# Optimization experiments

Hardware: AMD Instinct MI355X
Metric: run time of the kernel (lower is better)

Reference implementation:

```python
import jax, jax.numpy as jnp
import numpy as np

N, E, H, L, G = 50000, 500000, 128, 4, 1000
EPS = 1e-7      # GENConv message eps
LN_EPS = 1e-5   # torch LayerNorm default


def setup_inputs() -> dict:
    key = jax.random.key(0)
    ks = jax.random.split(key, 24)
    d = {}
    d["x"] = jax.random.normal(ks[0], (N, 9), jnp.float32)
    d["edge_index"] = jax.random.randint(ks[1], (2, E), 0, N, jnp.int32)
    d["edge_attr"] = jax.random.normal(ks[2], (E, 3), jnp.float32)
    d["batch"] = jnp.sort(jax.random.randint(ks[3], (N,), 0, G, jnp.int32))
    s9, s3, sh, s2h = 1/np.sqrt(9), 1/np.sqrt(3), 1/np.sqrt(H), 1/np.sqrt(2*H)
    u = lambda k, shp, s: jax.random.uniform(k, shp, jnp.float32, -s, s)
    d["enc_node_W"] = u(ks[4], (9, H), s9)
    d["enc_node_b"] = u(ks[5], (H,), s9)
    d["enc_edge_W"] = u(ks[6], (3, H), s3)
    d["enc_edge_b"] = u(ks[7], (H,), s3)
    d["ln_g"] = jnp.ones((L, H), jnp.float32)   # DeepGCNLayer pre-norm affine
    d["ln_b"] = jnp.zeros((L, H), jnp.float32)
    d["W1"] = u(ks[8], (L, H, 2*H), sh)          # GENConv MLP layer 1
    d["b1"] = u(ks[9], (L, 2*H), sh)
    d["mlp_ln_g"] = jnp.ones((L, 2*H), jnp.float32)
    d["mlp_ln_b"] = jnp.zeros((L, 2*H), jnp.float32)
    d["W2"] = u(ks[10], (L, 2*H, H), s2h)        # GENConv MLP layer 2
    d["b2"] = u(ks[11], (L, H), s2h)
    d["t"] = jnp.ones((L,), jnp.float32)         # learnable softmax temperature, init 1.0
    return d


def layernorm(x, g, b):
    mu = x.mean(-1, keepdims=True)
    var = ((x - mu) ** 2).mean(-1, keepdims=True)
    return (x - mu) / jnp.sqrt(var + LN_EPS) * g + b


def genconv(h, src, dst, ea, t, W1, b1, lg, lb, W2, b2):
    # message: relu(x_j + edge_attr) + eps   -> [E, H]
    msg = jax.nn.relu(h[src] + ea) + EPS
    # softmax aggregation over incoming edges, per channel
    logits = t * msg
    m = jax.ops.segment_max(logits, dst, num_segments=N)
    num = jnp.exp(logits - m[dst])
    den = jax.ops.segment_sum(num, dst, num_segments=N)
    alpha = num / den[dst]
    agg = jax.ops.segment_sum(msg * alpha, dst, num_segments=N)
    out = agg + h  # root residual inside GENConv
    z = jax.nn.relu(layernorm(out @ W1 + b1, lg, lb))
    return z @ W2 + b2


def reference(x, edge_index, edge_attr, batch, enc_node_W, enc_node_b,
              enc_edge_W, enc_edge_b, ln_g, ln_b, W1, b1, mlp_ln_g, mlp_ln_b,
              W2, b2, t):
    src, dst = edge_index[0], edge_index[1]
    h = x @ enc_node_W + enc_node_b            # node encoder  [N, H]
    ea = edge_attr @ enc_edge_W + enc_edge_b   # edge encoder  [E, H]
    # layer 0: conv only (DeeperGCN forward uses layers[0].conv directly)
    h = genconv(h, src, dst, ea, t[0], W1[0], b1[0], mlp_ln_g[0], mlp_ln_b[0], W2[0], b2[0])
    # layers 1..L-1: res+ block: x + conv(relu(LN(x))); dropout is identity (eval)
    for i in range(1, L):
        z = jax.nn.relu(layernorm(h, ln_g[i], ln_b[i]))
        h = h + genconv(z, src, dst, ea, t[i], W1[i], b1[i], mlp_ln_g[i], mlp_ln_b[i], W2[i], b2[i])
    h = jax.nn.relu(layernorm(h, ln_g[0], ln_b[0]))  # reuses layer-0 norm
    # global mean pool over graphs
    counts = jax.ops.segment_sum(jnp.ones((N,), h.dtype), batch, num_segments=G)
    sums = jax.ops.segment_sum(h, batch, num_segments=G)
    return sums / jnp.maximum(counts, 1.0)[:, None]
```

## Files before the change

### kernel.cpp

```cpp
#include <hip/hip_runtime.h>

#define NN 50000
#define NE 500000
#define HD 128
#define HD2 256
#define NL 4
#define NG 1000

constexpr float MSG_EPS = 1e-7f;
constexpr float LNEPS   = 1e-5f;

typedef float  f32x4  __attribute__((ext_vector_type(4)));
typedef float  f32x2  __attribute__((ext_vector_type(2)));
typedef __bf16 bf16x8 __attribute__((ext_vector_type(8)));

__device__ __forceinline__ unsigned short f2b(float f) {
    unsigned int u = __float_as_uint(f);
    unsigned int r = u + 0x7FFFu + ((u >> 16) & 1u);
    return (unsigned short)(r >> 16);
}
__device__ __forceinline__ float b2f(unsigned short h) {
    return __uint_as_float(((unsigned int)h) << 16);
}
__device__ __forceinline__ unsigned int pack2(float a, float b) {
    return (unsigned int)f2b(a) | ((unsigned int)f2b(b) << 16);
}

#define PREP_BLKS 512
#define ENC_BLKS 25000
#define HIST_BLKS ((NE + 255) / 256)

__global__ void k_setup(const float* __restrict__ x, const float* __restrict__ encW,
                        const float* __restrict__ encB, unsigned short* __restrict__ zb,
                        const float* __restrict__ W1, const float* __restrict__ W2,
                        unsigned short* __restrict__ W1T, unsigned short* __restrict__ W2T,
                        const int* __restrict__ dst, int* __restrict__ counts) {
    int bid = blockIdx.x, tid = threadIdx.x;
    if (bid < PREP_BLKS) {
        int idx = bid * 256 + tid;
        {
            int k = idx & 127, n = (idx >> 7) & 255, l = idx >> 15;
            W1T[idx] = f2b(W1[(l * 128 + k) * 256 + n]);
        }
        {
            int k = idx & 255, n = (idx >> 8) & 127, l = idx >> 15;
            W2T[idx] = f2b(W2[(l * 256 + k) * 128 + n]);
        }
    } else if (bid < PREP_BLKS + ENC_BLKS) {
        int n = (bid - PREP_BLKS) * 2 + (tid >> 7);
        int c = tid & 127;
        float xr[9];
#pragma unroll
        for (int k = 0; k < 9; k++) xr[k] = x[n * 9 + k];
        float acc = encB[c];
#pragma unroll
        for (int k = 0; k < 9; k++) acc = fmaf(xr[k], encW[k * HD + c], acc);
        zb[(size_t)n * HD + c] = f2b(acc);
    } else {
        int e = (bid - PREP_BLKS - ENC_BLKS) * 256 + tid;
        if (e < NE) atomicAdd(&counts[dst[e]], 1);
    }
}

#define SCAN_B 512
#define NSB ((NN + SCAN_B - 1) / SCAN_B)

__global__ void k_scan1(const int* __restrict__ counts, int* __restrict__ incl,
                        int* __restrict__ bsum) {
    __shared__ int s[SCAN_B];
    int i = blockIdx.x * SCAN_B + threadIdx.x;
    int v = (i < NN) ? counts[i] : 0;
    s[threadIdx.x] = v;
    __syncthreads();
    for (int off = 1; off < SCAN_B; off <<= 1) {
        int t = (threadIdx.x >= off) ? s[threadIdx.x - off] : 0;
        __syncthreads();
        s[threadIdx.x] += t;
        __syncthreads();
    }
    if (i < NN) incl[i] = s[threadIdx.x];
    if (threadIdx.x == SCAN_B - 1) bsum[blockIdx.x] = s[threadIdx.x];
}

__global__ void k_scan2(const int* __restrict__ bsum, int* __restrict__ boff, int nb) {
    __shared__ int s[128];
    int v = (threadIdx.x < nb) ? bsum[threadIdx.x] : 0;
    s[threadIdx.x] = v;
    __syncthreads();
    for (int off = 1; off < 128; off <<= 1) {
        int t = (threadIdx.x >= off) ? s[threadIdx.x - off] : 0;
        __syncthreads();
        s[threadIdx.x] += t;
        __syncthreads();
    }
    if (threadIdx.x < nb) boff[threadIdx.x] = s[threadIdx.x] - v;
}

__global__ void k_scan3g(const int* __restrict__ incl, const int* __restrict__ boff,
                         int* __restrict__ row_start, const int* __restrict__ batch,
                         int* __restrict__ gstart) {
    if (blockIdx.x < NSB) {
        int i = blockIdx.x * SCAN_B + threadIdx.x;
        if (i < NN) row_start[i + 1] = incl[i] + boff[blockIdx.x];
        if (i == 0) row_start[0] = 0;
    } else {
        int g = (blockIdx.x - NSB) * SCAN_B + threadIdx.x;
        if (g > NG) return;
        int lo = 0, hi = NN;
        while (lo < hi) {
            int mid = (lo + hi) >> 1;
            if (batch[mid] < g) lo = mid + 1;
            else hi = mid;
        }
        gstart[g] = lo;
    }
}

__global__ void k_scatter(const int* __restrict__ src, const int* __restrict__ dst,
                          const float* __restrict__ eattr, const int* __restrict__ row_start,
                          int* __restrict__ cursor, float4* __restrict__ aperm) {
    int e = blockIdx.x * blockDim.x + threadIdx.x;
    if (e >= NE) return;
    int d = dst[e];
    int p = row_start[d] + atomicAdd(&cursor[d], 1);
    float4 v;
    v.x = eattr[e * 3 + 0];
    v.y = eattr[e * 3 + 1];
    v.z = eattr[e * 3 + 2];
    v.w = __int_as_float(src[e]);
    aperm[p] = v;
}

__device__ __forceinline__ void edge_acc2(float4 a, unsigned int zz, f32x2 w0, f32x2 w1,
                                          f32x2 w2, f32x2 bb, float tv, f32x2& num,
                                          f32x2& wm) {
    f32x2 z;
    z.x = b2f((unsigned short)zz);
    z.y = b2f((unsigned short)(zz >> 16));
    f32x2 m = z + bb + a.x * w0 + a.y * w1 + a.z * w2;
    m.x = fmaxf(m.x, 0.f);
    m.y = fmaxf(m.y, 0.f);
    f32x2 tm = tv * m;
    f32x2 e;
    e.x = __expf(tm.x);
    e.y = __expf(tm.y);
    num += e;
    wm += m * e;
}

__global__ __launch_bounds__(256) void k_aggregate(const unsigned short* __restrict__ zbin,
                                                   const float4* __restrict__ aperm,
                                                   const int* __restrict__ row_start,
                                                   const float* __restrict__ We,
                                                   const float* __restrict__ be,
                                                   const float* __restrict__ t, int layer,
                                                   unsigned int* __restrict__ outb) {
    int w = threadIdx.x >> 6, lane = threadIdx.x & 63;
    int n = blockIdx.x * 4 + w;
    if (n >= NN) return;
    int c = lane * 2;
    f32x2 w0 = *(const f32x2*)&We[c];
    f32x2 w1 = *(const f32x2*)&We[HD + c];
    f32x2 w2 = *(const f32x2*)&We[2 * HD + c];
    f32x2 bb = *(const f32x2*)&be[c];
    float tv = t[layer];
    int s0 = row_start[n], s1 = row_start[n + 1];
    f32x2 num = (f32x2){0.f, 0.f}, wm = (f32x2){0.f, 0.f};
    const unsigned int* z32 = (const unsigned int*)zbin;
    int p = s0;
    for (; p + 8 <= s1; p += 8) {
        float4 A[8];
#pragma unroll
        for (int j = 0; j < 8; j++) A[j] = aperm[p + j];
        unsigned int Z[8];
#pragma unroll
        for (int j = 0; j < 8; j++) {
            int sj = __builtin_amdgcn_readfirstlane(__float_as_int(A[j].w));
            Z[j] = z32[(size_t)sj * 64 + lane];
        }
#pragma unroll
        for (int j = 0; j < 8; j++) edge_acc2(A[j], Z[j], w0, w1, w2, bb, tv, num, wm);
    }
    for (; p + 4 <= s1; p += 4) {
        float4 A[4];
#pragma unroll
        for (int j = 0; j < 4; j++) A[j] = aperm[p + j];
        unsigned int Z[4];
#pragma unroll
        for (int j = 0; j < 4; j++) {
            int sj = __builtin_amdgcn_readfirstlane(__float_as_int(A[j].w));
            Z[j] = z32[(size_t)sj * 64 + lane];
        }
#pragma unroll
        for (int j = 0; j < 4; j++) edge_acc2(A[j], Z[j], w0, w1, w2, bb, tv, num, wm);
    }
    for (; p < s1; p++) {
        float4 a = aperm[p];
        int sj = __builtin_amdgcn_readfirstlane(__float_as_int(a.w));
        unsigned int zz = z32[(size_t)sj * 64 + lane];
        edge_acc2(a, zz, w0, w1, w2, bb, tv, num, wm);
    }
    unsigned int zn = z32[(size_t)n * 64 + lane];
    bool has = s1 > s0;
    float ox = (has ? (wm.x / num.x + MSG_EPS) : 0.f) + b2f((unsigned short)zn);
    float oy = (has ? (wm.y / num.y + MSG_EPS) : 0.f) + b2f((unsigned short)(zn >> 16));
    outb[(size_t)n * 64 + lane] = pack2(ox, oy);
}

#define BM 32
#define HS_LD 264
#define HT_LD 136

__global__ __launch_bounds__(256) void k_mlp(const unsigned short* __restrict__ outb,
                                             const unsigned short* __restrict__ W1T,
                                             const float* __restrict__ b1l,
                                             const float* __restrict__ lgl,
                                             const float* __restrict__ lbl,
                                             const unsigned short* __restrict__ W2T,
                                             const float* __restrict__ b2l,
                                             unsigned short* __restrict__ h,
                                             const float* __restrict__ gn,
                                             const float* __restrict__ bn,
                                             unsigned short* __restrict__ zb,
                                             int add_residual) {
    __shared__ __align__(16) unsigned short Hs[BM * HS_LD];
    __shared__ __align__(16) unsigned short Ht[BM * HT_LD];
    __shared__ __align__(16) float2 st1[2][16][4];

    int nb = blockIdx.x * BM;
    int tid = threadIdx.x;
    int w = tid >> 6, lane = tid & 63, q = lane >> 4, i = lane & 15;

    f32x4 acc[2][4];
#pragma unroll
    for (int rt = 0; rt < 2; rt++)
#pragma unroll
        for (int ct = 0; ct < 4; ct++) acc[rt][ct] = (f32x4){0.f, 0.f, 0.f, 0.f};

    bf16x8 acur[2], bcur[4];
#pragma unroll
    for (int rt = 0; rt < 2; rt++) {
        int row = nb + rt * 16 + i;
        acur[rt] = (row < NN) ? *(const bf16x8*)&outb[(size_t)row * HD + q * 8]
                              : (bf16x8)(__bf16)0.f;
    }
#pragma unroll
    for (int ct = 0; ct < 4; ct++)
        bcur[ct] = *(const bf16x8*)&W1T[(w * 64 + ct * 16 + i) * HD + q * 8];

#pragma unroll
    for (int ks = 0; ks < 4; ks++) {
        bf16x8 anxt[2], bnxt[4];
        if (ks < 3) {
#pragma unroll
            for (int rt = 0; rt < 2; rt++) {
                int row = nb + rt * 16 + i;
                anxt[rt] = (row < NN)
                               ? *(const bf16x8*)&outb[(size_t)row * HD + (ks + 1) * 32 + q * 8]
                               : (bf16x8)(__bf16)0.f;
            }
#pragma unroll
            for (int ct = 0; ct < 4; ct++)
                bnxt[ct] =
                    *(const bf16x8*)&W1T[(w * 64 + ct * 16 + i) * HD + (ks + 1) * 32 + q * 8];
        }
#pragma unroll
        for (int rt = 0; rt < 2; rt++)
#pragma unroll
            for (int ct = 0; ct < 4; ct++)
                acc[rt][ct] =
                    __builtin_amdgcn_mfma_f32_16x16x32_bf16(acur[rt], bcur[ct], acc[rt][ct],
                                                            0, 0, 0);
        if (ks < 3) {
#pragma unroll
            for (int rt = 0; rt < 2; rt++) acur[rt] = anxt[rt];
#pragma unroll
            for (int ct = 0; ct < 4; ct++) bcur[ct] = bnxt[ct];
        }
    }

#pragma unroll
    for (int ct = 0; ct < 4; ct++) {
        float bb = b1l[w * 64 + ct * 16 + i];
#pragma unroll
        for (int rt = 0; rt < 2; rt++)
#pragma unroll
            for (int r = 0; r < 4; r++) acc[rt][ct][r] += bb;
    }

    {
        float sv[2][4], qv[2][4];
#pragma unroll
        for (int rt = 0; rt < 2; rt++)
#pragma unroll
            for (int r = 0; r < 4; r++) {
                float s = acc[rt][0][r] + acc[rt][1][r] + acc[rt][2][r] + acc[rt][3][r];
                float sq = 0.f;
#pragma unroll
                for (int ct = 0; ct < 4; ct++) sq = fmaf(acc[rt][ct][r], acc[rt][ct][r], sq);
                sv[rt][r] = s;
                qv[rt][r] = sq;
            }
#pragma unroll
        for (int m = 1; m <= 8; m <<= 1)
#pragma unroll
            for (int rt = 0; rt < 2; rt++)
#pragma unroll
                for (int r = 0; r < 4; r++) {
                    sv[rt][r] += __shfl_xor(sv[rt][r], m);
                    qv[rt][r] += __shfl_xor(qv[rt][r], m);
                }
        if (i == 0) {
#pragma unroll
            for (int rt = 0; rt < 2; rt++)
#pragma unroll
                for (int r = 0; r < 4; r++)
                    st1[rt][q * 4 + r][w] = make_float2(sv[rt][r], qv[rt][r]);
        }
    }
    __syncthreads();

    {
        float mu[2][4], inv[2][4];
#pragma unroll
        for (int rt = 0; rt < 2; rt++)
#pragma unroll
            for (int r = 0; r < 4; r++) {
                const float4* sp = (const float4*)&st1[rt][q * 4 + r][0];
                float4 a = sp[0], b = sp[1];
                float S = a.x + a.z + b.x + b.z;
                float Q = a.y + a.w + b.y + b.w;
                float m_ = S * (1.f / 256.f);
                float v_ = Q * (1.f / 256.f) - m_ * m_;
                mu[rt][r] = m_;
                inv[rt][r] = rsqrtf(v_ + LNEPS);
            }
#pragma unroll
        for (int ct = 0; ct < 4; ct++) {
            float g = lgl[w * 64 + ct * 16 + i];
            float c = lbl[w * 64 + ct * 16 + i];
#pragma unroll
            for (int rt = 0; rt < 2; rt++)
#pragma unroll
                for (int r = 0; r < 4; r++) {
                    float v =
                        fmaxf(fmaf((acc[rt][ct][r] - mu[rt][r]) * inv[rt][r], g, c), 0.f);
                    Hs[(rt * 16 + q * 4 + r) * HS_LD + w * 64 + ct * 16 + i] = f2b(v);
                }
        }
    }
    __syncthreads();

    f32x4 acc2[2][2];
#pragma unroll
    for (int rt = 0; rt < 2; rt++)
#pragma unroll
        for (int ct = 0; ct < 2; ct++) acc2[rt][ct] = (f32x4){0.f, 0.f, 0.f, 0.f};

    bf16x8 hc[2], bc[2];
#pragma unroll
    for (int rt = 0; rt < 2; rt++) hc[rt] = *(const bf16x8*)&Hs[(rt * 16 + i) * HS_LD + q * 8];
#pragma unroll
    for (int ct = 0; ct < 2; ct++)
        bc[ct] = *(const bf16x8*)&W2T[(w * 32 + ct * 16 + i) * HD2 + q * 8];

#pragma unroll
    for (int ks = 0; ks < 8; ks++) {
        bf16x8 hn[2], bn2[2];
        if (ks < 7) {
#pragma unroll
            for (int rt = 0; rt < 2; rt++)
                hn[rt] = *(const bf16x8*)&Hs[(rt * 16 + i) * HS_LD + (ks + 1) * 32 + q * 8];
#pragma unroll
            for (int ct = 0; ct < 2; ct++)
                bn2[ct] =
                    *(const bf16x8*)&W2T[(w * 32 + ct * 16 + i) * HD2 + (ks + 1) * 32 + q * 8];
        }
#pragma unroll
        for (int rt = 0; rt < 2; rt++)
#pragma unroll
            for (int ct = 0; ct < 2; ct++)
                acc2[rt][ct] = __builtin_amdgcn_mfma_f32_16x16x32_bf16(hc[rt], bc[ct],
                                                                      acc2[rt][ct], 0, 0, 0);
        if (ks < 7) {
#pragma unroll
            for (int rt = 0; rt < 2; rt++) hc[rt] = hn[rt];
#pragma unroll
            for (int ct = 0; ct < 2; ct++) bc[ct] = bn2[ct];
        }
    }

#pragma unroll
    for (int ct = 0; ct < 2; ct++) {
        float bb = b2l[w * 32 + ct * 16 + i];
#pragma unroll
        for (int rt = 0; rt < 2; rt++)
#pragma unroll
            for (int r = 0; r < 4; r++)
                Ht[(rt * 16 + q * 4 + r) * HT_LD + w * 32 + ct * 16 + i] =
                    f2b(acc2[rt][ct][r] + bb);
    }
    __syncthreads();

    {
        const unsigned int* Ht32 = (const unsigned int*)Ht;
        unsigned int* h32 = (unsigned int*)h;
        unsigned int* zb32 = (unsigned int*)zb;
        float2 gg = *(const float2*)&gn[lane * 2];
        float2 cc = *(const float2*)&bn[lane * 2];
        for (int rr = w; rr < BM; rr += 4) {
            int row = nb + rr;
            if (row >= NN) break;
            unsigned int tv = Ht32[rr * (HT_LD / 2) + lane];
            float cx = b2f((unsigned short)tv), cy = b2f((unsigned short)(tv >> 16));
            if (add_residual) {
                unsigned int hv = h32[(size_t)row * 64 + lane];
                cx += b2f((unsigned short)hv);
                cy += b2f((unsigned short)(hv >> 16));
            }
            h32[(size_t)row * 64 + lane] = pack2(cx, cy);
            float s = cx + cy, sq = cx * cx + cy * cy;
#pragma unroll
            for (int m = 32; m >= 1; m >>= 1) {
                s += __shfl_xor(s, m);
                sq += __shfl_xor(sq, m);
            }
            float mu = s * (1.f / 128.f);
            float var = sq * (1.f / 128.f) - mu * mu;
            float inv = rsqrtf(var + LNEPS);
            float z0 = fmaxf(fmaf((cx - mu) * inv, gg.x, cc.x), 0.f);
            float z1 = fmaxf(fmaf((cy - mu) * inv, gg.y, cc.y), 0.f);
            zb32[(size_t)row * 64 + lane] = pack2(z0, z1);
        }
    }
}

__global__ void k_pool(const unsigned short* __restrict__ zb, const int* __restrict__ gstart,
                       float* __restrict__ out) {
    int g = blockIdx.x;
    int c = threadIdx.x;
    int a = gstart[g], b = gstart[g + 1];
    float s0 = 0.f, s1 = 0.f;
    int n = a;
    for (; n + 2 <= b; n += 2) {
        s0 += b2f(zb[(size_t)n * HD + c]);
        s1 += b2f(zb[(size_t)(n + 1) * HD + c]);
    }
    if (n < b) s0 += b2f(zb[(size_t)n * HD + c]);
    out[g * HD + c] = (s0 + s1) / fmaxf((float)(b - a), 1.f);
}

extern "C" void kernel_launch(void* const* d_in, const int* in_sizes, int n_in, void* d_out,
                              int out_size, void* d_ws, size_t ws_size, hipStream_t stream) {
    const float* x     = (const float*)d_in[0];
    const int* ei      = (const int*)d_in[1];
    const float* eattr = (const float*)d_in[2];
    const int* batch   = (const int*)d_in[3];
    const float* encW  = (const float*)d_in[4];
    const float* encB  = (const float*)d_in[5];
    const float* eW    = (const float*)d_in[6];
    const float* eB    = (const float*)d_in[7];
    const float* ln_g  = (const float*)d_in[8];
    const float* ln_b  = (const float*)d_in[9];
    const float* W1    = (const float*)d_in[10];
    const float* b1    = (const float*)d_in[11];
    const float* mlg   = (const float*)d_in[12];
    const float* mlb   = (const float*)d_in[13];
    const float* W2    = (const float*)d_in[14];
    const float* b2    = (const float*)d_in[15];
    const float* t     = (const float*)d_in[16];
    const int* src = ei;
    const int* dst = ei + NE;

    char* w = (char*)d_ws;
    auto alloc = [&](size_t bytes) {
        char* p = w;
        w += (bytes + 255) & ~size_t(255);
        return p;
    };
    unsigned short* h    = (unsigned short*)alloc(sizeof(unsigned short) * NN * HD);
    unsigned short* zb   = (unsigned short*)alloc(sizeof(unsigned short) * NN * HD);
    unsigned int* outb   = (unsigned int*)alloc(sizeof(unsigned int) * NN * HD / 2);
    float4* aperm        = (float4*)alloc(sizeof(float4) * NE);
    int* row_start       = (int*)alloc(sizeof(int) * (NN + 1));
    int* counts          = (int*)alloc(sizeof(int) * NN);
    int* cursor          = (int*)alloc(sizeof(int) * NN);
    int* incl            = (int*)alloc(sizeof(int) * NN);
    int* bsum            = (int*)alloc(sizeof(int) * 128);
    int* boff            = (int*)alloc(sizeof(int) * 128);
    int* gstart          = (int*)alloc(sizeof(int) * (NG + 1));
    unsigned short* W1T  = (unsigned short*)alloc(sizeof(unsigned short) * NL * HD * HD2);
    unsigned short* W2T  = (unsigned short*)alloc(sizeof(unsigned short) * NL * HD2 * HD);

    hipMemsetAsync(counts, 0, sizeof(int) * NN, stream);
    hipMemsetAsync(cursor, 0, sizeof(int) * NN, stream);

    k_setup<<<PREP_BLKS + ENC_BLKS + HIST_BLKS, 256, 0, stream>>>(x, encW, encB, zb, W1, W2,
                                                                  W1T, W2T, dst, counts);
    k_scan1<<<NSB, SCAN_B, 0, stream>>>(counts, incl, bsum);
    k_scan2<<<1, 128, 0, stream>>>(bsum, boff, NSB);
    k_scan3g<<<NSB + 2, SCAN_B, 0, stream>>>(incl, boff, row_start, batch, gstart);
    k_scatter<<<(NE + 255) / 256, 256, 0, stream>>>(src, dst, eattr, row_start, cursor, aperm);

    for (int l = 0; l < NL; l++) {
        k_aggregate<<<(NN + 3) / 4, 256, 0, stream>>>(zb, aperm, row_start, eW, eB, t, l, outb);
        int ln_next = (l + 1) % NL;
        k_mlp<<<(NN + BM - 1) / BM, 256, 0, stream>>>(
            (const unsigned short*)outb, W1T + (size_t)l * HD * HD2, b1 + l * HD2,
            mlg + l * HD2, mlb + l * HD2, W2T + (size_t)l * HD2 * HD, b2 + l * HD, h,
            ln_g + ln_next * HD, ln_b + ln_next * HD, zb, l > 0);
    }
    k_pool<<<NG, HD, 0, stream>>>(zb, gstart, (float*)d_out);
}
```

Measured before the change: 509.1 us.

## Halve MLP row tile to 16 and streamline aggregate exp and bf16 unpack

The fused MLP kernel now processes 16 rows per block instead of 32. It drops the second row tile and the row-bound checks, since 50000 divides evenly by 16. This doubles the grid and cuts registers and LDS per block, aiming for higher occupancy at the cost of re-reading the weight tiles more often. The aggregate kernel folds log2e into the temperature to use exp2f, unpacks bf16 with shift and mask, and makes the row bounds wave-uniform via readfirstlane.

```diff
diff --git a/kernel.cpp b/kernel.cpp
--- a/kernel.cpp
+++ b/kernel.cpp
@@ -9,6 +9,7 @@
 
 constexpr float MSG_EPS = 1e-7f;
 constexpr float LNEPS   = 1e-5f;
+constexpr float LOG2E   = 1.4426950408889634f;
 
 typedef float  f32x4  __attribute__((ext_vector_type(4)));
 typedef float  f32x2  __attribute__((ext_vector_type(2)));
@@ -132,18 +133,17 @@
 }
 
 __device__ __forceinline__ void edge_acc2(float4 a, unsigned int zz, f32x2 w0, f32x2 w1,
-                                          f32x2 w2, f32x2 bb, float tv, f32x2& num,
+                                          f32x2 w2, f32x2 bb, float t2, f32x2& num,
                                           f32x2& wm) {
     f32x2 z;
-    z.x = b2f((unsigned short)zz);
-    z.y = b2f((unsigned short)(zz >> 16));
+    z.x = __uint_as_float(zz << 16);
+    z.y = __uint_as_float(zz & 0xFFFF0000u);
     f32x2 m = z + bb + a.x * w0 + a.y * w1 + a.z * w2;
     m.x = fmaxf(m.x, 0.f);
     m.y = fmaxf(m.y, 0.f);
-    f32x2 tm = tv * m;
     f32x2 e;
-    e.x = __expf(tm.x);
-    e.y = __expf(tm.y);
+    e.x = exp2f(t2 * m.x);
+    e.y = exp2f(t2 * m.y);
     num += e;
     wm += m * e;
 }
@@ -163,8 +163,9 @@
     f32x2 w1 = *(const f32x2*)&We[HD + c];
     f32x2 w2 = *(const f32x2*)&We[2 * HD + c];
     f32x2 bb = *(const f32x2*)&be[c];
-    float tv = t[layer];
-    int s0 = row_start[n], s1 = row_start[n + 1];
+    float t2 = t[layer] * LOG2E;
+    int s0 = __builtin_amdgcn_readfirstlane(row_start[n]);
+    int s1 = __builtin_amdgcn_readfirstlane(row_start[n + 1]);
     f32x2 num = (f32x2){0.f, 0.f}, wm = (f32x2){0.f, 0.f};
     const unsigned int* z32 = (const unsigned int*)zbin;
     int p = s0;
@@ -179,7 +180,7 @@
             Z[j] = z32[(size_t)sj * 64 + lane];
         }
 #pragma unroll
-        for (int j = 0; j < 8; j++) edge_acc2(A[j], Z[j], w0, w1, w2, bb, tv, num, wm);
+        for (int j = 0; j < 8; j++) edge_acc2(A[j], Z[j], w0, w1, w2, bb, t2, num, wm);
     }
     for (; p + 4 <= s1; p += 4) {
         float4 A[4];
@@ -192,22 +193,22 @@
             Z[j] = z32[(size_t)sj * 64 + lane];
         }
 #pragma unroll
-        for (int j = 0; j < 4; j++) edge_acc2(A[j], Z[j], w0, w1, w2, bb, tv, num, wm);
+        for (int j = 0; j < 4; j++) edge_acc2(A[j], Z[j], w0, w1, w2, bb, t2, num, wm);
     }
     for (; p < s1; p++) {
         float4 a = aperm[p];
         int sj = __builtin_amdgcn_readfirstlane(__float_as_int(a.w));
         unsigned int zz = z32[(size_t)sj * 64 + lane];
-        edge_acc2(a, zz, w0, w1, w2, bb, tv, num, wm);
+        edge_acc2(a, zz, w0, w1, w2, bb, t2, num, wm);
     }
     unsigned int zn = z32[(size_t)n * 64 + lane];
     bool has = s1 > s0;
-    float ox = (has ? (wm.x / num.x + MSG_EPS) : 0.f) + b2f((unsigned short)zn);
-    float oy = (has ? (wm.y / num.y + MSG_EPS) : 0.f) + b2f((unsigned short)(zn >> 16));
+    float ox = (has ? (wm.x / num.x + MSG_EPS) : 0.f) + __uint_as_float(zn << 16);
+    float oy = (has ? (wm.y / num.y + MSG_EPS) : 0.f) + __uint_as_float(zn & 0xFFFF0000u);
     outb[(size_t)n * 64 + lane] = pack2(ox, oy);
 }
 
-#define BM 32
+#define BM 16
 #define HS_LD 264
 #define HT_LD 136
 
@@ -225,55 +226,37 @@
                                              int add_residual) {
     __shared__ __align__(16) unsigned short Hs[BM * HS_LD];
     __shared__ __align__(16) unsigned short Ht[BM * HT_LD];
-    __shared__ __align__(16) float2 st1[2][16][4];
+    __shared__ __align__(16) float2 st1[16][4];
 
     int nb = blockIdx.x * BM;
     int tid = threadIdx.x;
     int w = tid >> 6, lane = tid & 63, q = lane >> 4, i = lane & 15;
 
-    f32x4 acc[2][4];
-#pragma unroll
-    for (int rt = 0; rt < 2; rt++)
-#pragma unroll
-        for (int ct = 0; ct < 4; ct++) acc[rt][ct] = (f32x4){0.f, 0.f, 0.f, 0.f};
-
-    bf16x8 acur[2], bcur[4];
-#pragma unroll
-    for (int rt = 0; rt < 2; rt++) {
-        int row = nb + rt * 16 + i;
-        acur[rt] = (row < NN) ? *(const bf16x8*)&outb[(size_t)row * HD + q * 8]
-                              : (bf16x8)(__bf16)0.f;
-    }
+    f32x4 acc[4];
+#pragma unroll
+    for (int ct = 0; ct < 4; ct++) acc[ct] = (f32x4){0.f, 0.f, 0.f, 0.f};
+
+    bf16x8 acur, bcur[4];
+    acur = *(const bf16x8*)&outb[(size_t)(nb + i) * HD + q * 8];
 #pragma unroll
     for (int ct = 0; ct < 4; ct++)
         bcur[ct] = *(const bf16x8*)&W1T[(w * 64 + ct * 16 + i) * HD + q * 8];
 
 #pragma unroll
     for (int ks = 0; ks < 4; ks++) {
-        bf16x8 anxt[2], bnxt[4];
+        bf16x8 anxt, bnxt[4];
         if (ks < 3) {
-#pragma unroll
-            for (int rt = 0; rt < 2; rt++) {
-                int row = nb + rt * 16 + i;
-                anxt[rt] = (row < NN)
-                               ? *(const bf16x8*)&outb[(size_t)row * HD + (ks + 1) * 32 + q * 8]
-                               : (bf16x8)(__bf16)0.f;
-            }
+            anxt = *(const bf16x8*)&outb[(size_t)(nb + i) * HD + (ks + 1) * 32 + q * 8];
 #pragma unroll
             for (int ct = 0; ct < 4; ct++)
                 bnxt[ct] =
                     *(const bf16x8*)&W1T[(w * 64 + ct * 16 + i) * HD + (ks + 1) * 32 + q * 8];
         }
 #pragma unroll
-        for (int rt = 0; rt < 2; rt++)
-#pragma unroll
-            for (int ct = 0; ct < 4; ct++)
-                acc[rt][ct] =
-                    __builtin_amdgcn_mfma_f32_16x16x32_bf16(acur[rt], bcur[ct], acc[rt][ct],
-                                                            0, 0, 0);
+        for (int ct = 0; ct < 4; ct++)
+            acc[ct] = __builtin_amdgcn_mfma_f32_16x16x32_bf16(acur, bcur[ct], acc[ct], 0, 0, 0);
         if (ks < 3) {
-#pragma unroll
-            for (int rt = 0; rt < 2; rt++) acur[rt] = anxt[rt];
+            acur = anxt;
 #pragma unroll
             for (int ct = 0; ct < 4; ct++) bcur[ct] = bnxt[ct];
         }
@@ -283,108 +266,84 @@
     for (int ct = 0; ct < 4; ct++) {
         float bb = b1l[w * 64 + ct * 16 + i];
 #pragma unroll
-        for (int rt = 0; rt < 2; rt++)
-#pragma unroll
-            for (int r = 0; r < 4; r++) acc[rt][ct][r] += bb;
+        for (int r = 0; r < 4; r++) acc[ct][r] += bb;
     }
 
     {
-        float sv[2][4], qv[2][4];
-#pragma unroll
-        for (int rt = 0; rt < 2; rt++)
+        float sv[4], qv[4];
+#pragma unroll
+        for (int r = 0; r < 4; r++) {
+            sv[r] = acc[0][r] + acc[1][r] + acc[2][r] + acc[3][r];
+            float sq = 0.f;
+#pragma unroll
+            for (int ct = 0; ct < 4; ct++) sq = fmaf(acc[ct][r], acc[ct][r], sq);
+            qv[r] = sq;
+        }
+#pragma unroll
+        for (int m = 1; m <= 8; m <<= 1)
 #pragma unroll
             for (int r = 0; r < 4; r++) {
-                float s = acc[rt][0][r] + acc[rt][1][r] + acc[rt][2][r] + acc[rt][3][r];
-                float sq = 0.f;
-#pragma unroll
-                for (int ct = 0; ct < 4; ct++) sq = fmaf(acc[rt][ct][r], acc[rt][ct][r], sq);
-                sv[rt][r] = s;
-                qv[rt][r] = sq;
+                sv[r] += __shfl_xor(sv[r], m);
+                qv[r] += __shfl_xor(qv[r], m);
             }
-#pragma unroll
-        for (int m = 1; m <= 8; m <<= 1)
-#pragma unroll
-            for (int rt = 0; rt < 2; rt++)
-#pragma unroll
-                for (int r = 0; r < 4; r++) {
-                    sv[rt][r] += __shfl_xor(sv[rt][r], m);
-                    qv[rt][r] += __shfl_xor(qv[rt][r], m);
-                }
         if (i == 0) {
 #pragma unroll
-            for (int rt = 0; rt < 2; rt++)
-#pragma unroll
-                for (int r = 0; r < 4; r++)
-                    st1[rt][q * 4 + r][w] = make_float2(sv[rt][r], qv[rt][r]);
+            for (int r = 0; r < 4; r++) st1[q * 4 + r][w] = make_float2(sv[r], qv[r]);
         }
     }
     __syncthreads();
 
     {
-        float mu[2][4], inv[2][4];
-#pragma unroll
-        for (int rt = 0; rt < 2; rt++)
-#pragma unroll
-            for (int r = 0; r < 4; r++) {
-                const float4* sp = (const float4*)&st1[rt][q * 4 + r][0];
-                float4 a = sp[0], b = sp[1];
-                float S = a.x + a.z + b.x + b.z;
-                float Q = a.y + a.w + b.y + b.w;
-                float m_ = S * (1.f / 256.f);
-                float v_ = Q * (1.f / 256.f) - m_ * m_;
-                mu[rt][r] = m_;
-                inv[rt][r] = rsqrtf(v_ + LNEPS);
-            }
+        float mu[4], inv[4];
+#pragma unroll
+        for (int r = 0; r < 4; r++) {
+            const float4* sp = (const float4*)&st1[q * 4 + r][0];
+            float4 a = sp[0], b = sp[1];
+            float S = a.x + a.z + b.x + b.z;
+            float Q = a.y + a.w + b.y + b.w;
+            float m_ = S * (1.f / 256.f);
+            float v_ = Q * (1.f / 256.f) - m_ * m_;
+            mu[r] = m_;
+            inv[r] = rsqrtf(v_ + LNEPS);
+        }
 #pragma unroll
         for (int ct = 0; ct < 4; ct++) {
             float g = lgl[w * 64 + ct * 16 + i];
             float c = lbl[w * 64 + ct * 16 + i];
 #pragma unroll
-            for (int rt = 0; rt < 2; rt++)
-#pragma unroll
-                for (int r = 0; r < 4; r++) {
-                    float v =
-                        fmaxf(fmaf((acc[rt][ct][r] - mu[rt][r]) * inv[rt][r], g, c), 0.f);
-                    Hs[(rt * 16 + q * 4 + r) * HS_LD + w * 64 + ct * 16 + i] = f2b(v);
-                }
+            for (int r = 0; r < 4; r++) {
+                float v = fmaxf(fmaf((acc[ct][r] - mu[r]) * inv[r], g, c), 0.f);
+                Hs[(q * 4 + r) * HS_LD + w * 64 + ct * 16 + i] = f2b(v);
+            }
         }
     }
     __syncthreads();
 
-    f32x4 acc2[2][2];
-#pragma unroll
-    for (int rt = 0; rt < 2; rt++)
-#pragma unroll
-        for (int ct = 0; ct < 2; ct++) acc2[rt][ct] = (f32x4){0.f, 0.f, 0.f, 0.f};
-
-    bf16x8 hc[2], bc[2];
-#pragma unroll
-    for (int rt = 0; rt < 2; rt++) hc[rt] = *(const bf16x8*)&Hs[(rt * 16 + i) * HS_LD + q * 8];
+    f32x4 acc2[2];
+#pragma unroll
+    for (int ct = 0; ct < 2; ct++) acc2[ct] = (f32x4){0.f, 0.f, 0.f, 0.f};
+
+    bf16x8 hc, bc[2];
+    hc = *(const bf16x8*)&Hs[i * HS_LD + q * 8];
 #pragma unroll
     for (int ct = 0; ct < 2; ct++)
         bc[ct] = *(const bf16x8*)&W2T[(w * 32 + ct * 16 + i) * HD2 + q * 8];
 
 #pragma unroll
     for (int ks = 0; ks < 8; ks++) {
-        bf16x8 hn[2], bn2[2];
+        bf16x8 hn, bn2[2];
         if (ks < 7) {
-#pragma unroll
-            for (int rt = 0; rt < 2; rt++)
-                hn[rt] = *(const bf16x8*)&Hs[(rt * 16 + i) * HS_LD + (ks + 1) * 32 + q * 8];
+            hn = *(const bf16x8*)&Hs[i * HS_LD + (ks + 1) * 32 + q * 8];
 #pragma unroll
             for (int ct = 0; ct < 2; ct++)
                 bn2[ct] =
                     *(const bf16x8*)&W2T[(w * 32 + ct * 16 + i) * HD2 + (ks + 1) * 32 + q * 8];
         }
 #pragma unroll
-        for (int rt = 0; rt < 2; rt++)
-#pragma unroll
-            for (int ct = 0; ct < 2; ct++)
-                acc2[rt][ct] = __builtin_amdgcn_mfma_f32_16x16x32_bf16(hc[rt], bc[ct],
-                                                                      acc2[rt][ct], 0, 0, 0);
+        for (int ct = 0; ct < 2; ct++)
+            acc2[ct] = __builtin_amdgcn_mfma_f32_16x16x32_bf16(hc, bc[ct], acc2[ct], 0, 0, 0);
         if (ks < 7) {
-#pragma unroll
-            for (int rt = 0; rt < 2; rt++) hc[rt] = hn[rt];
+            hc = hn;
 #pragma unroll
             for (int ct = 0; ct < 2; ct++) bc[ct] = bn2[ct];
         }
@@ -394,11 +353,8 @@
     for (int ct = 0; ct < 2; ct++) {
         float bb = b2l[w * 32 + ct * 16 + i];
 #pragma unroll
-        for (int rt = 0; rt < 2; rt++)
-#pragma unroll
-            for (int r = 0; r < 4; r++)
-                Ht[(rt * 16 + q * 4 + r) * HT_LD + w * 32 + ct * 16 + i] =
-                    f2b(acc2[rt][ct][r] + bb);
+        for (int r = 0; r < 4; r++)
+            Ht[(q * 4 + r) * HT_LD + w * 32 + ct * 16 + i] = f2b(acc2[ct][r] + bb);
     }
     __syncthreads();
 
@@ -408,9 +364,10 @@
         unsigned int* zb32 = (unsigned int*)zb;
         float2 gg = *(const float2*)&gn[lane * 2];
         float2 cc = *(const float2*)&bn[lane * 2];
-        for (int rr = w; rr < BM; rr += 4) {
+#pragma unroll
+        for (int k = 0; k < 4; k++) {
+            int rr = w * 4 + k;
             int row = nb + rr;
-            if (row >= NN) break;
             unsigned int tv = Ht32[rr * (HT_LD / 2) + lane];
             float cx = b2f((unsigned short)tv), cy = b2f((unsigned short)(tv >> 16));
             if (add_residual) {
@@ -505,7 +462,7 @@
     for (int l = 0; l < NL; l++) {
         k_aggregate<<<(NN + 3) / 4, 256, 0, stream>>>(zb, aperm, row_start, eW, eB, t, l, outb);
         int ln_next = (l + 1) % NL;
-        k_mlp<<<(NN + BM - 1) / BM, 256, 0, stream>>>(
+        k_mlp<<<NN / BM, 256, 0, stream>>>(
             (const unsigned short*)outb, W1T + (size_t)l * HD * HD2, b1 + l * HD2,
             mlg + l * HD2, mlb + l * HD2, W2T + (size_t)l * HD2 * HD, b2 + l * HD, h,
             ln_g + ln_next * HD, ln_b + ln_next * HD, zb, l > 0);
```

Result: slower. 555.4 us (+9.1%).
